# Performance work log

Hardware: AMD Instinct MI355X
Metric: run time of the kernel (lower is better)

Reference implementation:

```python
import jax, jax.numpy as jnp
import numpy as np

N_NODES = 100000
N_EDGES = 1600000
IN_DIM = 512
HEADS = 8
CH = 8
OUT_DIM = 64
NEG_SLOPE = 0.2


def gat_conv(x, src, dst, W, a_src, a_dst, b, n_nodes):
    """PyG-style GATConv (eval mode, add_self_loops handled by caller).
    x: [N, F]; W: [F, H, C]; a_src/a_dst: [H, C]; b: [H*C].
    """
    xh = jnp.einsum('nf,fhc->nhc', x, W)              # [N, H, C]
    al_src = jnp.sum(xh * a_src, axis=-1)              # [N, H]
    al_dst = jnp.sum(xh * a_dst, axis=-1)              # [N, H]
    e = jax.nn.leaky_relu(al_src[src] + al_dst[dst], NEG_SLOPE)  # [E, H]
    # segment softmax over edges grouped by destination node
    emax = jax.ops.segment_max(e, dst, num_segments=n_nodes)     # [N, H]
    ex = jnp.exp(e - emax[dst])
    den = jax.ops.segment_sum(ex, dst, num_segments=n_nodes)     # [N, H]
    alpha = ex / (den[dst] + 1e-16)                    # [E, H]
    msg = xh[src] * alpha[..., None]                   # [E, H, C]
    out = jax.ops.segment_sum(msg, dst, num_segments=n_nodes)    # [N, H, C]
    return out.reshape(n_nodes, -1) + b                # concat heads


def setup_inputs() -> dict:
    key = jax.random.key(0)
    ks = jax.random.split(key, 9)
    x = jax.random.normal(ks[0], (N_NODES, IN_DIM), dtype=jnp.float32)
    edge_index = jax.random.randint(ks[1], (2, N_EDGES), 0, N_NODES, dtype=jnp.int32)
    s1 = 1.0 / np.sqrt(IN_DIM)
    W1 = jax.random.normal(ks[2], (IN_DIM, HEADS, CH), dtype=jnp.float32) * s1
    a1_src = jax.random.normal(ks[3], (HEADS, CH), dtype=jnp.float32) * 0.1
    a1_dst = jax.random.normal(ks[4], (HEADS, CH), dtype=jnp.float32) * 0.1
    b1 = jnp.zeros((HEADS * CH,), dtype=jnp.float32)
    s2 = 1.0 / np.sqrt(HEADS * CH)
    W2 = jax.random.normal(ks[5], (HEADS * CH, 1, OUT_DIM), dtype=jnp.float32) * s2
    a2_src = jax.random.normal(ks[6], (1, OUT_DIM), dtype=jnp.float32) * 0.1
    a2_dst = jax.random.normal(ks[7], (1, OUT_DIM), dtype=jnp.float32) * 0.1
    b2 = jnp.zeros((OUT_DIM,), dtype=jnp.float32)
    return {"x": x, "edge_index": edge_index, "W1": W1, "a1_src": a1_src,
            "a1_dst": a1_dst, "b1": b1, "W2": W2, "a2_src": a2_src,
            "a2_dst": a2_dst, "b2": b2}


def reference(x, edge_index, W1, a1_src, a1_dst, b1, W2, a2_src, a2_dst, b2):
    n = x.shape[0]
    loops = jnp.arange(n, dtype=edge_index.dtype)
    src = jnp.concatenate([edge_index[0], loops])  # add self-loops (PyG default)
    dst = jnp.concatenate([edge_index[1], loops])
    # dropout layers are identity in eval mode
    h = jax.nn.relu(gat_conv(x, src, dst, W1, a1_src, a1_dst, b1, n))
    out = gat_conv(h, src, dst, W2, a2_src, a2_dst, b2, n)
    return jax.nn.log_softmax(out, axis=1)
```

## Files before the change

### kernel.cpp

```cpp
#include <hip/hip_runtime.h>
#include <cstddef>

#define NN 100000
#define NE 1600000
#define IN_DIM 512
#define NEG 0.2f
#define HBLK 521
#define DEGMAX 64

typedef short bf16x8 __attribute__((ext_vector_type(8)));
typedef float f32x4 __attribute__((ext_vector_type(4)));

__device__ __forceinline__ unsigned short f2bf_rne(float f) {
    unsigned u = __builtin_bit_cast(unsigned, f);
    unsigned r = u + 0x7fffu + ((u >> 16) & 1u);
    return (unsigned short)(r >> 16);
}
__device__ __forceinline__ float bf2f(unsigned short h) {
    unsigned u = ((unsigned)h) << 16;
    return __builtin_bit_cast(float, u);
}

__global__ void k_pre(int* __restrict__ cnt,
                      const float* __restrict__ W1, unsigned short* __restrict__ h1,
                      unsigned short* __restrict__ l1,
                      const float* __restrict__ W2, unsigned short* __restrict__ h2,
                      unsigned short* __restrict__ l2) {
    int t = blockIdx.x * blockDim.x + threadIdx.x;
    if (t < NN) cnt[t] = 0;
    if (t < 64 * IN_DIM) {
        int n = t >> 9, k = t & 511;
        float v = W1[k * 64 + n];
        unsigned short h = f2bf_rne(v);
        h1[t] = h;
        l1[t] = f2bf_rne(v - bf2f(h));
    }
    if (t < 64 * 64) {
        int n = t >> 6, k = t & 63;
        float v = W2[k * 64 + n];
        unsigned short h = f2bf_rne(v);
        h2[t] = h;
        l2[t] = f2bf_rne(v - bf2f(h));
    }
}

template <int K, int NH, bool ABF16>
__global__ __launch_bounds__(256, 2) void k_mm_mfma(const void* __restrict__ Ap,
                                                    const unsigned short* __restrict__ Bhi,
                                                    const unsigned short* __restrict__ Blo,
                                                    unsigned short* __restrict__ outbf,
                                                    const float* __restrict__ asv,
                                                    const float* __restrict__ adv,
                                                    float* __restrict__ alsrc,
                                                    float* __restrict__ aldst,
                                                    const int* __restrict__ srcv,
                                                    const int* __restrict__ dstv,
                                                    int* __restrict__ cnt,
                                                    int* __restrict__ csr,
                                                    int fillBlocks) {
    __shared__ __align__(16) unsigned char aRaw[2][64 * 64 * 4];
    __shared__ __align__(16) unsigned short bHi[2][64 * 64];
    __shared__ __align__(16) unsigned short bLo[2][64 * 64];
    int tid = threadIdx.x;
    int mmIdx = blockIdx.x;
    if (fillBlocks > 0) {
        if (((blockIdx.x & 3) == 3) && ((blockIdx.x >> 2) < fillBlocks)) {
            int stride = fillBlocks * 256;
            for (int e = (blockIdx.x >> 2) * 256 + tid; e < NE; e += stride) {
                int d = dstv[e];
                int pos = atomicAdd(&cnt[d], 1);
                if (pos < DEGMAX) csr[(size_t)d * DEGMAX + pos] = srcv[e];
            }
            return;
        }
        int below = (blockIdx.x + 1) >> 2;
        if (below > fillBlocks) below = fillBlocks;
        mmIdx = blockIdx.x - below;
    }
    const int NCH = K / 64;
    int wave = tid >> 6, lane = tid & 63;
    int ln = lane & 15, kg = lane >> 4;
    int brow = mmIdx * 64;
    int r = wave * 16 + ln;
    const float* Af = (const float*)Ap;
    const unsigned short* Ab = (const unsigned short*)Ap;
    f32x4 acc[4] = {};

    auto stage = [&](int c, int buf) {
        if (!ABF16) {
            #pragma unroll
            for (int q = 0; q < 4; ++q) {
                int d = q * 256 + tid;
                int row = d >> 4;
                int s = (d & 15) ^ (row & 15);
                int grow = brow + row;
                if (grow >= NN) grow = NN - 1;
                const float* gp = Af + (size_t)grow * K + c * 64 + s * 4;
                __builtin_amdgcn_global_load_lds(
                    (const __attribute__((address_space(1))) float*)gp,
                    (__attribute__((address_space(3))) float*)((float*)&aRaw[buf][0] + (size_t)d * 4),
                    16, 0, 0);
            }
        } else {
            #pragma unroll
            for (int q = 0; q < 2; ++q) {
                int d = q * 256 + tid;
                int row = d >> 3;
                int s = (d & 7) ^ (row & 7);
                int grow = brow + row;
                if (grow >= NN) grow = NN - 1;
                const unsigned short* gp = Ab + (size_t)grow * K + c * 64 + s * 8;
                __builtin_amdgcn_global_load_lds(
                    (const __attribute__((address_space(1))) unsigned short*)gp,
                    (__attribute__((address_space(3))) unsigned short*)((unsigned short*)&aRaw[buf][0] + (size_t)d * 8),
                    16, 0, 0);
            }
        }
        #pragma unroll
        for (int q = 0; q < 2; ++q) {
            int d = q * 256 + tid;
            int row = d >> 3;
            int s = (d & 7) ^ (row & 7);
            const unsigned short* gh = Bhi + (size_t)row * K + c * 64 + s * 8;
            const unsigned short* gl = Blo + (size_t)row * K + c * 64 + s * 8;
            __builtin_amdgcn_global_load_lds(
                (const __attribute__((address_space(1))) unsigned short*)gh,
                (__attribute__((address_space(3))) unsigned short*)(&bHi[buf][(size_t)d * 8]),
                16, 0, 0);
            __builtin_amdgcn_global_load_lds(
                (const __attribute__((address_space(1))) unsigned short*)gl,
                (__attribute__((address_space(3))) unsigned short*)(&bLo[buf][(size_t)d * 8]),
                16, 0, 0);
        }
    };

    stage(0, 0);
    __syncthreads();
    for (int c = 0; c < NCH; ++c) {
        int buf = c & 1;
        if (c + 1 < NCH) stage(c + 1, buf ^ 1);
        #pragma unroll
        for (int sub = 0; sub < 2; ++sub) {
            int kg8 = sub * 4 + kg;
            bf16x8 ah, al;
            if (!ABF16) {
                int s0 = kg8 * 2;
                const float* base = (const float*)&aRaw[buf][0] + (size_t)r * 64;
                float4 f0 = *reinterpret_cast<const float4*>(base + ((s0) ^ (r & 15)) * 4);
                float4 f1 = *reinterpret_cast<const float4*>(base + ((s0 + 1) ^ (r & 15)) * 4);
                float xs[8] = {f0.x, f0.y, f0.z, f0.w, f1.x, f1.y, f1.z, f1.w};
                #pragma unroll
                for (int j = 0; j < 8; ++j) {
                    unsigned short h = f2bf_rne(xs[j]);
                    ah[j] = (short)h;
                    al[j] = (short)f2bf_rne(xs[j] - bf2f(h));
                }
            } else {
                int slotA = kg8 ^ (r & 7);
                ah = *reinterpret_cast<const bf16x8*>(
                    (const unsigned short*)&aRaw[buf][0] + (size_t)r * 64 + slotA * 8);
            }
            #pragma unroll
            for (int nt = 0; nt < 4; ++nt) {
                int rowB = nt * 16 + ln;
                int slotB = kg8 ^ (rowB & 7);
                bf16x8 bh = *reinterpret_cast<const bf16x8*>(&bHi[buf][rowB * 64 + slotB * 8]);
                bf16x8 bl = *reinterpret_cast<const bf16x8*>(&bLo[buf][rowB * 64 + slotB * 8]);
                acc[nt] = __builtin_amdgcn_mfma_f32_16x16x32_bf16(ah, bh, acc[nt], 0, 0, 0);
                if (!ABF16)
                    acc[nt] = __builtin_amdgcn_mfma_f32_16x16x32_bf16(al, bh, acc[nt], 0, 0, 0);
                acc[nt] = __builtin_amdgcn_mfma_f32_16x16x32_bf16(ah, bl, acc[nt], 0, 0, 0);
            }
        }
        __syncthreads();
    }
    int rbase = brow + wave * 16 + kg * 4;
    #pragma unroll
    for (int nt = 0; nt < 4; ++nt)
        #pragma unroll
        for (int i = 0; i < 4; ++i) {
            int rw = rbase + i;
            if (rw < NN) outbf[(size_t)rw * 64 + nt * 16 + ln] = f2bf_rne(acc[nt][i]);
        }
    if (NH == 8) {
        #pragma unroll
        for (int nt = 0; nt < 4; ++nt) {
            float as = asv[nt * 16 + ln], ad = adv[nt * 16 + ln];
            #pragma unroll
            for (int i = 0; i < 4; ++i) {
                float ps = acc[nt][i] * as;
                float pd = acc[nt][i] * ad;
                ps += __shfl_xor(ps, 1, 64); pd += __shfl_xor(pd, 1, 64);
                ps += __shfl_xor(ps, 2, 64); pd += __shfl_xor(pd, 2, 64);
                ps += __shfl_xor(ps, 4, 64); pd += __shfl_xor(pd, 4, 64);
                if ((lane & 7) == 0) {
                    int row = rbase + i;
                    if (row < NN) {
                        int head = nt * 2 + (ln >> 3);
                        alsrc[row * 8 + head] = ps;
                        aldst[row * 8 + head] = pd;
                    }
                }
            }
        }
    } else {
        #pragma unroll
        for (int i = 0; i < 4; ++i) {
            float ps = 0.f, pd = 0.f;
            #pragma unroll
            for (int nt = 0; nt < 4; ++nt) {
                ps += acc[nt][i] * asv[nt * 16 + ln];
                pd += acc[nt][i] * adv[nt * 16 + ln];
            }
            ps += __shfl_xor(ps, 1, 64); pd += __shfl_xor(pd, 1, 64);
            ps += __shfl_xor(ps, 2, 64); pd += __shfl_xor(pd, 2, 64);
            ps += __shfl_xor(ps, 4, 64); pd += __shfl_xor(pd, 4, 64);
            ps += __shfl_xor(ps, 8, 64); pd += __shfl_xor(pd, 8, 64);
            if ((lane & 15) == 0) {
                int row = rbase + i;
                if (row < NN) {
                    alsrc[row] = ps;
                    aldst[row] = pd;
                }
            }
        }
    }
}

__global__ void k_agg1(const unsigned short* __restrict__ xh, const float* __restrict__ alsrc,
                       const float* __restrict__ aldst, const int* __restrict__ cnt,
                       const int* __restrict__ csr, const float* __restrict__ b1,
                       unsigned short* __restrict__ hout) {
    int node = blockIdx.x * 4 + (threadIdx.x >> 6);
    int lane = threadIdx.x & 63;
    if (node >= NN) return;
    int h = lane >> 3;
    float adst = aldst[node * 8 + h];
    float es = alsrc[node * 8 + h] + adst;
    es = es >= 0.f ? es : NEG * es;
    float mA = es, dA = 1.f, aA = bf2f(xh[(size_t)node * 64 + lane]);
    float mB = -3e38f, dB = 0.f, aB = 0.f;
    int beg = node * DEGMAX;
    int deg = cnt[node];
    if (deg > DEGMAX) deg = DEGMAX;
    int end = beg + deg;
    int j = beg;

    auto upd4 = [&](int s0, int s1, int s2, int s3, float& m, float& d, float& a) {
        float e0 = alsrc[s0 * 8 + h] + adst;
        float e1 = alsrc[s1 * 8 + h] + adst;
        float e2 = alsrc[s2 * 8 + h] + adst;
        float e3 = alsrc[s3 * 8 + h] + adst;
        e0 = e0 >= 0.f ? e0 : NEG * e0;
        e1 = e1 >= 0.f ? e1 : NEG * e1;
        e2 = e2 >= 0.f ? e2 : NEG * e2;
        e3 = e3 >= 0.f ? e3 : NEG * e3;
        float v0 = bf2f(xh[(size_t)s0 * 64 + lane]);
        float v1 = bf2f(xh[(size_t)s1 * 64 + lane]);
        float v2 = bf2f(xh[(size_t)s2 * 64 + lane]);
        float v3 = bf2f(xh[(size_t)s3 * 64 + lane]);
        float nm = fmaxf(fmaxf(fmaxf(e0, e1), fmaxf(e2, e3)), m);
        float sc = __expf(m - nm);
        float w0 = __expf(e0 - nm), w1 = __expf(e1 - nm);
        float w2 = __expf(e2 - nm), w3 = __expf(e3 - nm);
        d = d * sc + (w0 + w1) + (w2 + w3);
        a = a * sc + (w0 * v0 + w1 * v1) + (w2 * v2 + w3 * v3);
        m = nm;
    };

    if (j + 7 < end) {
        int i0 = csr[j], i1 = csr[j + 1], i2 = csr[j + 2], i3 = csr[j + 3];
        int i4 = csr[j + 4], i5 = csr[j + 5], i6 = csr[j + 6], i7 = csr[j + 7];
        j += 8;
        for (; j + 7 < end; j += 8) {
            int n0 = csr[j], n1 = csr[j + 1], n2 = csr[j + 2], n3 = csr[j + 3];
            int n4 = csr[j + 4], n5 = csr[j + 5], n6 = csr[j + 6], n7 = csr[j + 7];
            upd4(i0, i1, i2, i3, mA, dA, aA);
            upd4(i4, i5, i6, i7, mB, dB, aB);
            i0 = n0; i1 = n1; i2 = n2; i3 = n3;
            i4 = n4; i5 = n5; i6 = n6; i7 = n7;
        }
        upd4(i0, i1, i2, i3, mA, dA, aA);
        upd4(i4, i5, i6, i7, mB, dB, aB);
    }
    for (; j + 3 < end; j += 4)
        upd4(csr[j], csr[j + 1], csr[j + 2], csr[j + 3], mA, dA, aA);
    for (; j < end; ++j) {
        int s = csr[j];
        float e = alsrc[s * 8 + h] + adst;
        e = e >= 0.f ? e : NEG * e;
        float xv = bf2f(xh[(size_t)s * 64 + lane]);
        float nm = fmaxf(mA, e);
        float sc = __expf(mA - nm);
        float w = __expf(e - nm);
        dA = dA * sc + w;
        aA = aA * sc + w * xv;
        mA = nm;
    }
    {
        float nm = fmaxf(mA, mB);
        float sA = __expf(mA - nm), sB = __expf(mB - nm);
        dA = dA * sA + dB * sB;
        aA = aA * sA + aB * sB;
    }
    float r = aA / (dA + 1e-16f) + b1[lane];
    hout[(size_t)node * 64 + lane] = f2bf_rne(fmaxf(r, 0.f));
}

__global__ void k_agg2(const unsigned short* __restrict__ xh, const float* __restrict__ alsrc,
                       const float* __restrict__ aldst, const int* __restrict__ cnt,
                       const int* __restrict__ csr, const float* __restrict__ b2,
                       float* __restrict__ out) {
    int node = blockIdx.x * 4 + (threadIdx.x >> 6);
    int lane = threadIdx.x & 63;
    if (node >= NN) return;
    float adst = aldst[node];
    float es = alsrc[node] + adst;
    es = es >= 0.f ? es : NEG * es;
    float mA = es, dA = 1.f, aA = bf2f(xh[(size_t)node * 64 + lane]);
    float mB = -3e38f, dB = 0.f, aB = 0.f;
    int beg = node * DEGMAX;
    int deg = cnt[node];
    if (deg > DEGMAX) deg = DEGMAX;
    int end = beg + deg;
    int j = beg;

    auto upd4 = [&](int s0, int s1, int s2, int s3, float& m, float& d, float& a) {
        float e0 = alsrc[s0] + adst;
        float e1 = alsrc[s1] + adst;
        float e2 = alsrc[s2] + adst;
        float e3 = alsrc[s3] + adst;
        e0 = e0 >= 0.f ? e0 : NEG * e0;
        e1 = e1 >= 0.f ? e1 : NEG * e1;
        e2 = e2 >= 0.f ? e2 : NEG * e2;
        e3 = e3 >= 0.f ? e3 : NEG * e3;
        float v0 = bf2f(xh[(size_t)s0 * 64 + lane]);
        float v1 = bf2f(xh[(size_t)s1 * 64 + lane]);
        float v2 = bf2f(xh[(size_t)s2 * 64 + lane]);
        float v3 = bf2f(xh[(size_t)s3 * 64 + lane]);
        float nm = fmaxf(fmaxf(fmaxf(e0, e1), fmaxf(e2, e3)), m);
        float sc = __expf(m - nm);
        float w0 = __expf(e0 - nm), w1 = __expf(e1 - nm);
        float w2 = __expf(e2 - nm), w3 = __expf(e3 - nm);
        d = d * sc + (w0 + w1) + (w2 + w3);
        a = a * sc + (w0 * v0 + w1 * v1) + (w2 * v2 + w3 * v3);
        m = nm;
    };

    if (j + 7 < end) {
        int i0 = csr[j], i1 = csr[j + 1], i2 = csr[j + 2], i3 = csr[j + 3];
        int i4 = csr[j + 4], i5 = csr[j + 5], i6 = csr[j + 6], i7 = csr[j + 7];
        j += 8;
        for (; j + 7 < end; j += 8) {
            int n0 = csr[j], n1 = csr[j + 1], n2 = csr[j + 2], n3 = csr[j + 3];
            int n4 = csr[j + 4], n5 = csr[j + 5], n6 = csr[j + 6], n7 = csr[j + 7];
            upd4(i0, i1, i2, i3, mA, dA, aA);
            upd4(i4, i5, i6, i7, mB, dB, aB);
            i0 = n0; i1 = n1; i2 = n2; i3 = n3;
            i4 = n4; i5 = n5; i6 = n6; i7 = n7;
        }
        upd4(i0, i1, i2, i3, mA, dA, aA);
        upd4(i4, i5, i6, i7, mB, dB, aB);
    }
    for (; j + 3 < end; j += 4)
        upd4(csr[j], csr[j + 1], csr[j + 2], csr[j + 3], mA, dA, aA);
    for (; j < end; ++j) {
        int s = csr[j];
        float e = alsrc[s] + adst;
        e = e >= 0.f ? e : NEG * e;
        float xv = bf2f(xh[(size_t)s * 64 + lane]);
        float nm = fmaxf(mA, e);
        float sc = __expf(mA - nm);
        float w = __expf(e - nm);
        dA = dA * sc + w;
        aA = aA * sc + w * xv;
        mA = nm;
    }
    {
        float nm = fmaxf(mA, mB);
        float sA = __expf(mA - nm), sB = __expf(mB - nm);
        dA = dA * sA + dB * sB;
        aA = aA * sA + aB * sB;
    }
    float v = aA / (dA + 1e-16f) + b2[lane];
    float mx = v;
    #pragma unroll
    for (int off = 1; off < 64; off <<= 1) mx = fmaxf(mx, __shfl_xor(mx, off, 64));
    float ex = __expf(v - mx);
    float s = ex;
    #pragma unroll
    for (int off = 1; off < 64; off <<= 1) s += __shfl_xor(s, off, 64);
    out[(size_t)node * 64 + lane] = v - mx - __logf(s);
}

extern "C" void kernel_launch(void* const* d_in, const int* in_sizes, int n_in,
                              void* d_out, int out_size, void* d_ws, size_t ws_size,
                              hipStream_t stream) {
    const float* x   = (const float*)d_in[0];
    const int*   ei  = (const int*)d_in[1];
    const float* W1  = (const float*)d_in[2];
    const float* a1s = (const float*)d_in[3];
    const float* a1d = (const float*)d_in[4];
    const float* b1  = (const float*)d_in[5];
    const float* W2  = (const float*)d_in[6];
    const float* a2s = (const float*)d_in[7];
    const float* a2d = (const float*)d_in[8];
    const float* b2  = (const float*)d_in[9];
    float* out = (float*)d_out;
    const int* srcv = ei;
    const int* dstv = ei + NE;

    char* w = (char*)d_ws;
    auto alloc = [&](size_t bytes) {
        void* p = (void*)w;
        w += (bytes + 255) & ~(size_t)255;
        return p;
    };
    unsigned short* xh1 = (unsigned short*)alloc((size_t)NN * 64 * 2);
    unsigned short* hbuf = (unsigned short*)alloc((size_t)NN * 64 * 2);
    float* al1s  = (float*)alloc((size_t)NN * 8 * 4);
    float* al1d  = (float*)alloc((size_t)NN * 8 * 4);
    float* al2s  = (float*)alloc((size_t)NN * 4);
    float* al2d  = (float*)alloc((size_t)NN * 4);
    int* cnt     = (int*)alloc((size_t)NN * 4);
    int* csr     = (int*)alloc((size_t)NN * DEGMAX * 4);
    unsigned short* Wb1h = (unsigned short*)alloc((size_t)64 * IN_DIM * 2);
    unsigned short* Wb1l = (unsigned short*)alloc((size_t)64 * IN_DIM * 2);
    unsigned short* Wb2h = (unsigned short*)alloc((size_t)64 * 64 * 2);
    unsigned short* Wb2l = (unsigned short*)alloc((size_t)64 * 64 * 2);
    unsigned short* xh2 = xh1;

    const int MMB = (NN + 63) / 64;

    k_pre<<<(NN + 255) / 256, 256, 0, stream>>>(cnt, W1, Wb1h, Wb1l, W2, Wb2h, Wb2l);

    k_mm_mfma<IN_DIM, 8, false><<<MMB + HBLK, 256, 0, stream>>>(x, Wb1h, Wb1l, xh1,
                                                                a1s, a1d, al1s, al1d,
                                                                srcv, dstv, cnt, csr, HBLK);

    k_agg1<<<(NN + 3) / 4, 256, 0, stream>>>(xh1, al1s, al1d, cnt, csr, b1, hbuf);

    k_mm_mfma<64, 1, true><<<MMB, 256, 0, stream>>>(hbuf, Wb2h, Wb2l, xh2,
                                                    a2s, a2d, al2s, al2d,
                                                    srcv, dstv, cnt, csr, 0);
    k_agg2<<<(NN + 3) / 4, 256, 0, stream>>>(xh2, al2s, al2d, cnt, csr, b2, out);
}
```

Before: 320.3 us.

## Fuse layer-2 projection and attention logits into layer-1 aggregation kernel

Removes the separate layer-2 MFMA matmul launch and the intermediate hidden buffer round trip. Each agg1 block now loads W2 (16 KB) into shared memory, computes the 64x64 projection per node from the relu'd, bf16-rounded hidden row, writes the bf16 xh2, and reduces the src/dst attention logits with wave shuffles. In exchange every block reloads W2 and does scalar FMA work instead of MFMA, and the early-return bounds check is dropped because a __syncthreads now follows, which relies on NN being divisible by 4.

After: 340.4 us. 6.3% more time.

```diff
diff --git a/kernel.cpp b/kernel.cpp
--- a/kernel.cpp
+++ b/kernel.cpp
@@ -23,9 +23,7 @@
 
 __global__ void k_pre(int* __restrict__ cnt,
                       const float* __restrict__ W1, unsigned short* __restrict__ h1,
-                      unsigned short* __restrict__ l1,
-                      const float* __restrict__ W2, unsigned short* __restrict__ h2,
-                      unsigned short* __restrict__ l2) {
+                      unsigned short* __restrict__ l1) {
     int t = blockIdx.x * blockDim.x + threadIdx.x;
     if (t < NN) cnt[t] = 0;
     if (t < 64 * IN_DIM) {
@@ -34,13 +32,6 @@
         unsigned short h = f2bf_rne(v);
         h1[t] = h;
         l1[t] = f2bf_rne(v - bf2f(h));
-    }
-    if (t < 64 * 64) {
-        int n = t >> 6, k = t & 63;
-        float v = W2[k * 64 + n];
-        unsigned short h = f2bf_rne(v);
-        h2[t] = h;
-        l2[t] = f2bf_rne(v - bf2f(h));
     }
 }
 
@@ -203,37 +194,23 @@
                 }
             }
         }
-    } else {
-        #pragma unroll
-        for (int i = 0; i < 4; ++i) {
-            float ps = 0.f, pd = 0.f;
-            #pragma unroll
-            for (int nt = 0; nt < 4; ++nt) {
-                ps += acc[nt][i] * asv[nt * 16 + ln];
-                pd += acc[nt][i] * adv[nt * 16 + ln];
-            }
-            ps += __shfl_xor(ps, 1, 64); pd += __shfl_xor(pd, 1, 64);
-            ps += __shfl_xor(ps, 2, 64); pd += __shfl_xor(pd, 2, 64);
-            ps += __shfl_xor(ps, 4, 64); pd += __shfl_xor(pd, 4, 64);
-            ps += __shfl_xor(ps, 8, 64); pd += __shfl_xor(pd, 8, 64);
-            if ((lane & 15) == 0) {
-                int row = rbase + i;
-                if (row < NN) {
-                    alsrc[row] = ps;
-                    aldst[row] = pd;
-                }
-            }
-        }
     }
 }
 
 __global__ void k_agg1(const unsigned short* __restrict__ xh, const float* __restrict__ alsrc,
                        const float* __restrict__ aldst, const int* __restrict__ cnt,
                        const int* __restrict__ csr, const float* __restrict__ b1,
-                       unsigned short* __restrict__ hout) {
-    int node = blockIdx.x * 4 + (threadIdx.x >> 6);
-    int lane = threadIdx.x & 63;
-    if (node >= NN) return;
+                       const float* __restrict__ W2, const float* __restrict__ a2s,
+                       const float* __restrict__ a2d,
+                       unsigned short* __restrict__ xh2,
+                       float* __restrict__ al2s, float* __restrict__ al2d) {
+    __shared__ float w2s[64 * 64];
+    __shared__ float hsh[4][64];
+    int tid = threadIdx.x;
+    #pragma unroll
+    for (int q = 0; q < 16; ++q) w2s[q * 256 + tid] = W2[q * 256 + tid];
+    int node = blockIdx.x * 4 + (tid >> 6);
+    int lane = tid & 63;
     int h = lane >> 3;
     float adst = aldst[node * 8 + h];
     float es = alsrc[node * 8 + h] + adst;
@@ -304,7 +281,21 @@
         aA = aA * sA + aB * sB;
     }
     float r = aA / (dA + 1e-16f) + b1[lane];
-    hout[(size_t)node * 64 + lane] = f2bf_rne(fmaxf(r, 0.f));
+    r = fmaxf(r, 0.f);
+    hsh[tid >> 6][lane] = bf2f(f2bf_rne(r));
+    __syncthreads();
+    float o = 0.f;
+    const float* hr = hsh[tid >> 6];
+    #pragma unroll 8
+    for (int k = 0; k < 64; ++k) o += hr[k] * w2s[k * 64 + lane];
+    xh2[(size_t)node * 64 + lane] = f2bf_rne(o);
+    float ps = o * a2s[lane], pd = o * a2d[lane];
+    #pragma unroll
+    for (int off = 1; off < 64; off <<= 1) {
+        ps += __shfl_xor(ps, off, 64);
+        pd += __shfl_xor(pd, off, 64);
+    }
+    if (lane == 0) { al2s[node] = ps; al2d[node] = pd; }
 }
 
 __global__ void k_agg2(const unsigned short* __restrict__ xh, const float* __restrict__ alsrc,
@@ -417,7 +408,7 @@
         return p;
     };
     unsigned short* xh1 = (unsigned short*)alloc((size_t)NN * 64 * 2);
-    unsigned short* hbuf = (unsigned short*)alloc((size_t)NN * 64 * 2);
+    unsigned short* xh2 = (unsigned short*)alloc((size_t)NN * 64 * 2);
     float* al1s  = (float*)alloc((size_t)NN * 8 * 4);
     float* al1d  = (float*)alloc((size_t)NN * 8 * 4);
     float* al2s  = (float*)alloc((size_t)NN * 4);
@@ -426,22 +417,17 @@
     int* csr     = (int*)alloc((size_t)NN * DEGMAX * 4);
     unsigned short* Wb1h = (unsigned short*)alloc((size_t)64 * IN_DIM * 2);
     unsigned short* Wb1l = (unsigned short*)alloc((size_t)64 * IN_DIM * 2);
-    unsigned short* Wb2h = (unsigned short*)alloc((size_t)64 * 64 * 2);
-    unsigned short* Wb2l = (unsigned short*)alloc((size_t)64 * 64 * 2);
-    unsigned short* xh2 = xh1;
 
     const int MMB = (NN + 63) / 64;
 
-    k_pre<<<(NN + 255) / 256, 256, 0, stream>>>(cnt, W1, Wb1h, Wb1l, W2, Wb2h, Wb2l);
+    k_pre<<<(NN + 255) / 256, 256, 0, stream>>>(cnt, W1, Wb1h, Wb1l);
 
     k_mm_mfma<IN_DIM, 8, false><<<MMB + HBLK, 256, 0, stream>>>(x, Wb1h, Wb1l, xh1,
                                                                 a1s, a1d, al1s, al1d,
                                                                 srcv, dstv, cnt, csr, HBLK);
 
-    k_agg1<<<(NN + 3) / 4, 256, 0, stream>>>(xh1, al1s, al1d, cnt, csr, b1, hbuf);
-
-    k_mm_mfma<64, 1, true><<<MMB, 256, 0, stream>>>(hbuf, Wb2h, Wb2l, xh2,
-                                                    a2s, a2d, al2s, al2d,
-                                                    srcv, dstv, cnt, csr, 0);
-    k_agg2<<<(NN + 3) / 4, 256, 0, stream>>>(xh2, al2s, al2d, cnt, csr, b2, out);
-}
+    k_agg1<<<NN / 4, 256, 0, stream>>>(xh1, al1s, al1d, cnt, csr, b1,
+                                       W2, a2s, a2d, xh2, al2s, al2d);
+
+    k_agg2<<<NN / 4, 256, 0, stream>>>(xh2, al2s, al2d, cnt, csr, b2, out);
+}
```
